# Kernel tuning notes

Hardware: AMD Instinct MI355X
Metric: run time of the kernel (lower is better)

Reference implementation:

```python
import jax, jax.numpy as jnp
import numpy as np
from jax import lax

G, DS, RANK, K = 4, 16, 8, 4  # num_groups, d_state, dt_rank, conv kernel


def setup_inputs() -> dict:
    key = jax.random.key(0)
    B, C, L = 8, 512, 2048
    D = C // G      # per-group dim = 128
    E = 2 * D       # mamba d_inner (expand=2) = 256
    ks = jax.random.split(key, 12)
    rn = lambda k, shape, s=0.02: jax.random.normal(k, shape, jnp.float32) * s
    return {
        "x": jax.random.normal(ks[0], (B, C, L), jnp.float32),
        "gamma": jnp.ones((C,), jnp.float32),
        "beta": jnp.zeros((C,), jnp.float32),
        "cam_w1": rn(ks[1], (C // 4, C)),
        "cam_b1": jnp.zeros((C // 4,), jnp.float32),
        "cam_w2": rn(ks[2], (C, C // 4)),
        "cam_b2": jnp.zeros((C,), jnp.float32),
        "Win": rn(ks[3], (G, 2 * E, D)),
        "convw": rn(ks[4], (G, E, K), 0.1),
        "convb": jnp.zeros((G, E), jnp.float32),
        "Wxp": rn(ks[5], (G, RANK + 2 * DS, E)),
        "Wdt": rn(ks[6], (G, E, RANK), 0.1),
        "bdt": jnp.full((G, E), -4.6, jnp.float32),  # softplus(-4.6) ~ 0.01
        "Alog": jnp.log(jnp.broadcast_to(jnp.arange(1, DS + 1, dtype=jnp.float32), (G, E, DS))),
        "Dp": jnp.ones((G, E), jnp.float32),
        "Wout": rn(ks[7], (G, D, E)),
        "proj_w": rn(ks[8], (C, C)),
        "proj_b": jnp.zeros((C,), jnp.float32),
    }


def _vss_block(x, Win, convw, convb, Wxp, Wdt, bdt, Alog, Dp, Wout):
    """Mamba-style selective-scan block. x: (B, D, L) for one channel group."""
    Bsz, D, L = x.shape
    E = Win.shape[0] // 2
    S = Alog.shape[1]
    xz = jnp.einsum('ed,bdl->bel', Win, x)           # (B, 2E, L)
    xp, z = jnp.split(xz, 2, axis=1)
    # causal depthwise conv (kernel K)
    xpad = jnp.pad(xp, ((0, 0), (0, 0), (K - 1, 0)))
    xc = lax.conv_general_dilated(xpad, convw[:, None, :], (1,), 'VALID',
                                  feature_group_count=E,
                                  dimension_numbers=('NCH', 'OIH', 'NCH'))
    xc = jax.nn.silu(xc + convb[None, :, None])      # (B, E, L)
    xdbl = jnp.einsum('re,bel->brl', Wxp, xc)        # (B, R+2S, L)
    dt_low = xdbl[:, :RANK]
    Bc = xdbl[:, RANK:RANK + S]                      # (B, S, L)
    Cc = xdbl[:, RANK + S:]                          # (B, S, L)
    dt = jax.nn.softplus(jnp.einsum('er,brl->bel', Wdt, dt_low) + bdt[None, :, None])
    A = -jnp.exp(Alog)                               # (E, S)

    def step(h, inp):
        dt_t, B_t, C_t, x_t = inp                    # (B,E),(B,S),(B,S),(B,E)
        h = jnp.exp(dt_t[..., None] * A) * h + (dt_t * x_t)[..., None] * B_t[:, None, :]
        y = jnp.einsum('bes,bs->be', h, C_t)
        return h, y

    seq = (dt.transpose(2, 0, 1), Bc.transpose(2, 0, 1),
           Cc.transpose(2, 0, 1), xc.transpose(2, 0, 1))
    h0 = jnp.zeros((Bsz, E, S), x.dtype)
    _, ys = lax.scan(step, h0, seq)                  # (L, B, E)
    y = ys.transpose(1, 2, 0) + Dp[None, :, None] * xc
    y = y * jax.nn.silu(z)
    return jnp.einsum('de,bel->bdl', Wout, y)        # back to (B, D, L)


def reference(x, gamma, beta, cam_w1, cam_b1, cam_w2, cam_b2, Win, convw, convb,
              Wxp, Wdt, bdt, Alog, Dp, Wout, proj_w, proj_b):
    residual = x
    # LayerNorm over channel dim (torch: transpose -> LN(d_model) -> transpose)
    mu = jnp.mean(x, axis=1, keepdims=True)
    var = jnp.var(x, axis=1, keepdims=True)
    xn = (x - mu) * lax.rsqrt(var + 1e-5) * gamma[None, :, None] + beta[None, :, None]
    # channel attention (CAM): global avg pool over L, two 1x1 convs, sigmoid
    pooled = jnp.mean(xn, axis=2)                                    # (B, C)
    w = jax.nn.sigmoid(jax.nn.relu(pooled @ cam_w1.T + cam_b1) @ cam_w2.T + cam_b2)
    B_, C, L = x.shape
    D = C // G
    xg = xn.reshape(B_, G, D, L).transpose(1, 0, 2, 3)               # (G, B, D, L)
    outs = jax.vmap(_vss_block)(xg, Win, convw, convb, Wxp, Wdt, bdt, Alog, Dp, Wout)
    y = outs.transpose(1, 0, 2, 3).reshape(B_, C, L)                 # concat groups
    y = y * w[:, :, None]
    y = jnp.einsum('oc,bcl->bol', proj_w, y) + proj_b[None, :, None]  # 1x1 conv proj
    return y + residual
```

## Files before the change

kernel.cpp:

```cpp
#include <hip/hip_runtime.h>
#include <hip/hip_bf16.h>
#include <math.h>

#define B_  8
#define C_  512
#define L_  2048
#define G_  4
#define D_  128
#define E_  256
#define S_  16
#define NC_ 64
#define LC_ 32
#define CH_ 128

typedef __hip_bfloat16 bf16;
typedef __attribute__((ext_vector_type(4))) unsigned short ushort4_t;
typedef __attribute__((ext_vector_type(8))) short short8_t;
typedef __attribute__((ext_vector_type(4))) float f32x4;

__device__ __forceinline__ float b2f(bf16 v) { return __bfloat162float(v); }
__device__ __forceinline__ bf16  f2b(float v) { return __float2bfloat16(v); }
__device__ __forceinline__ float us2f(unsigned short u) {
    union { unsigned int i; float f; } c; c.i = ((unsigned int)u) << 16; return c.f;
}
__device__ __forceinline__ unsigned short f2us(float v) {
    bf16 b = f2b(v); return *(unsigned short*)&b;
}

#define OFFB_XN     0ull
#define OFFB_XPC    16777216ull
#define OFFB_XDBL   50331648ull
#define OFFB_HCH    60817408ull
#define OFFB_HALO   78643200ull
#define OFFB_WINB   78692352ull
#define OFFB_WOUTB  79216640ull
#define OFFB_PROJB  79478784ull
#define OFFB_SSUM   80003072ull
#define OFFB_SSQ    80068608ull
#define OFFB_POOL   80134144ull
#define OFFB_W      80150528ull
#define OFFB_DTSUM  0ull
#define OFFB_HALOT  4194304ull

__device__ __forceinline__ float softplusf(float x) {
    return (x > 20.f) ? x : __logf(1.f + __expf(x));
}
__device__ __forceinline__ float sigmoidf_(float x) {
    return 1.f / (1.f + __expf(-x));
}

__global__ __launch_bounds__(256) void k_cast3(const float* __restrict__ w1,
                                               const float* __restrict__ w2,
                                               const float* __restrict__ w3,
                                               bf16* __restrict__ dst) {
    int i = blockIdx.x * 256 + threadIdx.x;
    float v;
    if (i < 262144)      v = w1[i];
    else if (i < 393216) v = w2[i - 262144];
    else                 v = w3[i - 393216];
    dst[i] = f2b(v);
}

__global__ __launch_bounds__(256) void k_ln_stats(const float* __restrict__ x,
                                                  float* __restrict__ ssum,
                                                  float* __restrict__ ssq) {
    const int t = threadIdx.x;
    const int l = blockIdx.x * 256 + t;
    const int c0 = blockIdx.y * 64;
    const int b = blockIdx.z;
    const float* xb = x + (size_t)b * C_ * L_;
    float s = 0.f, q = 0.f;
    #pragma unroll 8
    for (int cc = 0; cc < 64; ++cc) {
        float v = xb[(size_t)(c0 + cc) * L_ + l];
        s += v; q = fmaf(v, v, q);
    }
    atomicAdd(&ssum[b * L_ + l], s);
    atomicAdd(&ssq[b * L_ + l], q);
}

__global__ __launch_bounds__(256) void k_ln_apply(const float* __restrict__ x,
                                                  const float* __restrict__ ssum,
                                                  const float* __restrict__ ssq,
                                                  const float* __restrict__ gamma,
                                                  const float* __restrict__ beta,
                                                  bf16* __restrict__ xn,
                                                  float* __restrict__ pooled) {
    __shared__ float red[256];
    const int t = threadIdx.x;
    const int blk = blockIdx.x;
    const int b = blk >> 9, c = blk & 511;
    const float gm = gamma[c], bt = beta[c];
    const float* xb = x + ((size_t)b * C_ + c) * L_;
    bf16* xnb = xn + ((size_t)b * C_ + c) * L_;
    const float* smb = ssum + b * L_;
    const float* sqb = ssq + b * L_;
    float pacc = 0.f;
    #pragma unroll
    for (int qq = 0; qq < 8; ++qq) {
        const int l = qq * 256 + t;
        const float sm = smb[l], sq = sqb[l];
        const float mu = sm * (1.f / C_);
        const float var = sq * (1.f / C_) - mu * mu;
        const float rs = rsqrtf(var + 1e-5f);
        const float v = (xb[l] - mu) * rs * gm + bt;
        xnb[l] = f2b(v);
        pacc += v;
    }
    red[t] = pacc;
    __syncthreads();
    #pragma unroll
    for (int off = 128; off; off >>= 1) {
        if (t < off) red[t] += red[t + off];
        __syncthreads();
    }
    if (t == 0) pooled[b * C_ + c] = red[0] * (1.f / L_);
}

__global__ __launch_bounds__(256) void k_cam(const float* __restrict__ pooled,
                                             const float* __restrict__ w1,
                                             const float* __restrict__ b1,
                                             const float* __restrict__ w2,
                                             const float* __restrict__ b2,
                                             float* __restrict__ wv) {
    __shared__ float ps[C_];
    __shared__ float h1[128];
    const int b = blockIdx.x, tid = threadIdx.x;
    ps[tid]       = pooled[b * C_ + tid];
    ps[tid + 256] = pooled[b * C_ + tid + 256];
    __syncthreads();
    if (tid < 128) {
        float acc = b1[tid];
        for (int c = 0; c < C_; ++c) acc = fmaf(w1[tid * C_ + c], ps[c], acc);
        h1[tid] = fmaxf(acc, 0.f);
    }
    __syncthreads();
    #pragma unroll
    for (int t = 0; t < 2; ++t) {
        int o = tid + t * 256;
        float acc = b2[o];
        for (int r = 0; r < 128; ++r) acc = fmaf(w2[o * 128 + r], h1[r], acc);
        wv[b * C_ + o] = sigmoidf_(acc);
    }
}

__global__ __launch_bounds__(256) void k_tr_act(const unsigned short* __restrict__ in,
                                                unsigned short* __restrict__ outp,
                                                int R) {
    __shared__ unsigned short tl[64][68];
    const int t = threadIdx.x;
    const int c0 = blockIdx.x * 64;
    const int r0 = blockIdx.y * 64;
    const size_t pofs = (size_t)blockIdx.z * R * 2048;
    const unsigned short* ip = in + pofs;
    unsigned short* op = outp + pofs;
    const int rr = t >> 4, c4 = (t & 15) * 4;
    #pragma unroll
    for (int q = 0; q < 4; ++q) {
        const int row = q * 16 + rr;
        *(ushort4_t*)&tl[row][c4] =
            *(const ushort4_t*)&ip[(size_t)(r0 + row) * 2048 + c0 + c4];
    }
    __syncthreads();
    #pragma unroll
    for (int q = 0; q < 4; ++q) {
        const int cr = q * 16 + rr;
        ushort4_t v;
        v.x = tl[c4 + 0][cr]; v.y = tl[c4 + 1][cr];
        v.z = tl[c4 + 2][cr]; v.w = tl[c4 + 3][cr];
        *(ushort4_t*)&op[(size_t)(c0 + cr) * R + r0 + c4] = v;
    }
}

template <int KD, typename EPI>
__device__ __forceinline__ void mma_tile(const bf16* __restrict__ W,
                                         const bf16* __restrict__ XT,
                                         const int m0, const int l0, EPI epi) {
    __shared__ __align__(16) short Asm[128][40];
    __shared__ __align__(16) short Xsm[128][40];
    const int tid = threadIdx.x;
    const int row = tid >> 1, kh = (tid & 1) * 16;
    const int lane = tid & 63, wid = tid >> 6;
    const int wm = (wid & 1) * 64, wl = (wid >> 1) * 64;
    const int lm = lane & 15, quad = lane >> 4;
    const short* Wg = (const short*)W;
    const short* Xg = (const short*)XT;
    f32x4 acc[4][4];
    #pragma unroll
    for (int i = 0; i < 4; ++i)
        #pragma unroll
        for (int j = 0; j < 4; ++j) acc[i][j] = (f32x4){0.f, 0.f, 0.f, 0.f};

    for (int k0 = 0; k0 < KD; k0 += 32) {
        __syncthreads();
        *(short8_t*)&Asm[row][kh]     = *(const short8_t*)&Wg[(size_t)(m0 + row) * KD + k0 + kh];
        *(short8_t*)&Asm[row][kh + 8] = *(const short8_t*)&Wg[(size_t)(m0 + row) * KD + k0 + kh + 8];
        *(short8_t*)&Xsm[row][kh]     = *(const short8_t*)&Xg[(size_t)(l0 + row) * KD + k0 + kh];
        *(short8_t*)&Xsm[row][kh + 8] = *(const short8_t*)&Xg[(size_t)(l0 + row) * KD + k0 + kh + 8];
        __syncthreads();
        short8_t af[4], bfr[4];
        #pragma unroll
        for (int i = 0; i < 4; ++i)
            af[i] = *(const short8_t*)&Asm[wm + i * 16 + lm][quad * 8];
        #pragma unroll
        for (int j = 0; j < 4; ++j)
            bfr[j] = *(const short8_t*)&Xsm[wl + j * 16 + lm][quad * 8];
        #pragma unroll
        for (int i = 0; i < 4; ++i)
            #pragma unroll
            for (int j = 0; j < 4; ++j)
                acc[i][j] = __builtin_amdgcn_mfma_f32_16x16x32_bf16(af[i], bfr[j], acc[i][j], 0, 0, 0);
    }
    #pragma unroll
    for (int i = 0; i < 4; ++i) {
        #pragma unroll
        for (int j = 0; j < 4; ++j) {
            #pragma unroll
            for (int r = 0; r < 4; ++r) {
                const int m = m0 + wm + i * 16 + quad * 4 + r;
                const int l = l0 + wl + j * 16 + lm;
                epi(m, l, acc[i][j][r]);
            }
        }
    }
}

__global__ __launch_bounds__(256) void k_mm_win(const bf16* __restrict__ winB,
                                                const bf16* __restrict__ xnT,
                                                bf16* __restrict__ xpT,
                                                bf16* __restrict__ zT) {
    const int m0 = blockIdx.x * 128;
    const int l0 = blockIdx.y * 128;
    const int bg = blockIdx.z, g = bg & 3;
    const bf16* A  = xnT + (size_t)bg * L_ * 128;
    const bf16* Bt = winB + (size_t)g * 512 * 128;
    unsigned short* xpb = (unsigned short*)xpT + (size_t)bg * L_ * E_;
    unsigned short* zb  = (unsigned short*)zT  + (size_t)bg * L_ * E_;
    mma_tile<128>(A, Bt, m0, l0,
                  [&](int lr, int ec, float v) {
                      if (ec < 256) xpb[(size_t)lr * E_ + ec] = f2us(v);
                      else          zb[(size_t)lr * E_ + (ec - 256)] = f2us(v);
                  });
}

__global__ __launch_bounds__(256) void k_mm_wout(const bf16* __restrict__ woutB,
                                                 const bf16* __restrict__ yT,
                                                 const float* __restrict__ wvec,
                                                 bf16* __restrict__ scaledT) {
    const int m0 = blockIdx.x * 128;
    const int bg = blockIdx.z, b = bg >> 2, g = bg & 3;
    const bf16* A  = yT + (size_t)bg * L_ * E_;
    const bf16* Bt = woutB + (size_t)g * 128 * 256;
    unsigned short* Outp = (unsigned short*)scaledT + (size_t)b * L_ * C_;
    const float* wrow = wvec + b * C_ + g * D_;
    mma_tile<256>(A, Bt, m0, 0,
                  [&](int lr, int dc, float v) {
                      Outp[(size_t)lr * C_ + g * D_ + dc] = f2us(v * wrow[dc]);
                  });
}

__global__ __launch_bounds__(256) void k_mm_proj(const bf16* __restrict__ projB,
                                                 const bf16* __restrict__ scaledT,
                                                 const float* __restrict__ pb,
                                                 const float* __restrict__ xres,
                                                 float* __restrict__ outp) {
    const int l0 = blockIdx.x * 128, m0 = blockIdx.y * 128;
    const int b = blockIdx.z;
    const bf16* XT = scaledT + (size_t)b * L_ * C_;
    const float* xr = xres + (size_t)b * C_ * L_;
    float* Outp = outp + (size_t)b * C_ * L_;
    mma_tile<512>(projB, XT, m0, l0,
                  [&](int m, int l, float v) {
                      Outp[(size_t)m * L_ + l] = v + pb[m] + xr[(size_t)m * L_ + l];
                  });
}

__global__ __launch_bounds__(256) void k_halo(const bf16* __restrict__ xpT,
                                              bf16* __restrict__ halo) {
    const int c = blockIdx.x, bg = blockIdx.y, e = threadIdx.x;
    if (c == 0) return;
    const unsigned short* src = (const unsigned short*)xpT +
                                ((size_t)bg * L_ + c * CH_ - 3) * E_ + e;
    unsigned short* dst = (unsigned short*)halo + ((size_t)(bg * 16 + c) * 3) * E_ + e;
    #pragma unroll
    for (int j = 0; j < 3; ++j) dst[j * E_] = src[(size_t)j * E_];
}

__global__ __launch_bounds__(256) void k_conv(bf16* __restrict__ xpT,
                                              const bf16* __restrict__ halo,
                                              const float* __restrict__ convw,
                                              const float* __restrict__ convb) {
    const int c = blockIdx.x, bg = blockIdx.y;
    const int e = threadIdx.x;
    const int g = bg & 3;
    const int ge = g * E_ + e;
    unsigned short* row = (unsigned short*)xpT + ((size_t)bg * L_ + c * CH_) * E_ + e;
    float x3, x2, x1;
    if (c == 0) { x3 = 0.f; x2 = 0.f; x1 = 0.f; }
    else {
        const unsigned short* hp = (const unsigned short*)halo +
                                   ((size_t)(bg * 16 + c) * 3) * E_ + e;
        x3 = us2f(hp[0]); x2 = us2f(hp[E_]); x1 = us2f(hp[2 * E_]);
    }
    const float w0 = convw[ge * 4 + 0], w1 = convw[ge * 4 + 1],
                w2 = convw[ge * 4 + 2], w3 = convw[ge * 4 + 3];
    const float bb = convb[ge];
    #pragma unroll 4
    for (int l = 0; l < CH_; ++l) {
        const float xv = us2f(row[(size_t)l * E_]);
        float acc = bb;
        acc = fmaf(w0, x3, acc);
        acc = fmaf(w1, x2, acc);
        acc = fmaf(w2, x1, acc);
        acc = fmaf(w3, xv, acc);
        row[(size_t)l * E_] = f2us(acc * sigmoidf_(acc));
        x3 = x2; x2 = x1; x1 = xv;
    }
}

__global__ __launch_bounds__(256) void k_xdbl(const float* __restrict__ Wxp,
                                              const bf16* __restrict__ xcT,
                                              float* __restrict__ xdbl) {
    __shared__ unsigned short xs[32][258];
    __shared__ float wsm[40][256];
    const int tid = threadIdx.x;
    const int l0 = blockIdx.x * 32;
    const int bg = blockIdx.y;
    const int g = bg & 3;
    const float* wsrc = Wxp + g * (40 * 256);
    for (int i = tid; i < 40 * 256; i += 256) wsm[i >> 8][i & 255] = wsrc[i];
    const unsigned short* xcu = (const unsigned short*)xcT + ((size_t)bg * L_ + l0) * E_;
    #pragma unroll
    for (int it = 0; it < 16; ++it) {
        const int flat = it * 256 + tid;
        const int li = flat >> 7, e2 = (flat & 127) * 2;
        *(unsigned int*)&xs[li][e2] = *(const unsigned int*)&xcu[(size_t)li * E_ + e2];
    }
    __syncthreads();
    const int li = tid & 31, rg = tid >> 5;
    float acc[5];
    #pragma unroll
    for (int j = 0; j < 5; ++j) acc[j] = 0.f;
    for (int k4 = 0; k4 < 64; ++k4) {
        const int k = k4 * 4;
        const float xv0 = us2f(xs[li][k + 0]);
        const float xv1 = us2f(xs[li][k + 1]);
        const float xv2 = us2f(xs[li][k + 2]);
        const float xv3 = us2f(xs[li][k + 3]);
        #pragma unroll
        for (int j = 0; j < 5; ++j) {
            const float4 wq = *reinterpret_cast<const float4*>(&wsm[rg * 5 + j][k]);
            acc[j] = fmaf(wq.x, xv0, fmaf(wq.y, xv1, fmaf(wq.z, xv2, fmaf(wq.w, xv3, acc[j]))));
        }
    }
    float* ob = xdbl + ((size_t)bg * L_ + l0 + li) * 40 + rg * 5;
    #pragma unroll
    for (int j = 0; j < 5; ++j) ob[j] = acc[j];
}

__global__ __launch_bounds__(256) void k_scanA(const float* __restrict__ xdbl,
                                               const bf16* __restrict__ xcT,
                                               const float* __restrict__ Wdt,
                                               const float* __restrict__ bdt,
                                               const float* __restrict__ Alog,
                                               bf16* __restrict__ hch,
                                               float* __restrict__ dtsum) {
    __shared__ float ts[LC_][28];
    const int tid = threadIdx.x;
    const int blk = blockIdx.x;
    const int bg = blk >> 6, ch = blk & 63;
    const int g = bg & 3;
    const int l0 = ch * LC_;
    const int eg = tid;

    const unsigned short* xr = (const unsigned short*)xcT +
                               ((size_t)bg * L_ + l0) * E_ + eg;
    unsigned short xcur[8], xnxt[8];
    #pragma unroll
    for (int k = 0; k < 8; ++k) xcur[k] = xr[(size_t)k * E_];

    float wdtv[8];
    #pragma unroll
    for (int r = 0; r < 8; ++r) wdtv[r] = Wdt[(g * E_ + eg) * 8 + r];
    const float bde = bdt[g * E_ + eg];
    const float a0 = -__expf(Alog[(g * E_ + eg) * 16]);

    {
        const float* xd = xdbl + ((size_t)bg * L_ + l0) * 40;
        const int li = tid & 31, r0 = (tid >> 5) * 3;
        #pragma unroll
        for (int r = 0; r < 3; ++r) ts[li][r0 + r] = xd[(size_t)li * 40 + r0 + r];
    }
    __syncthreads();

    float h[16];
    #pragma unroll
    for (int s = 0; s < 16; ++s) h[s] = 0.f;
    float dsum = 0.f;

    #pragma unroll 1
    for (int qw = 0; qw < 4; ++qw) {
        if (qw < 3) {
            const unsigned short* xp2 = xr + (size_t)(qw + 1) * 8 * E_;
            #pragma unroll
            for (int k = 0; k < 8; ++k) xnxt[k] = xp2[(size_t)k * E_];
        }
        #pragma unroll
        for (int k = 0; k < 8; ++k) {
            const int i = qw * 8 + k;
            const float4 d0 = *reinterpret_cast<const float4*>(&ts[i][0]);
            const float4 d1 = *reinterpret_cast<const float4*>(&ts[i][4]);
            float dtp = bde;
            dtp = fmaf(wdtv[0], d0.x, dtp); dtp = fmaf(wdtv[1], d0.y, dtp);
            dtp = fmaf(wdtv[2], d0.z, dtp); dtp = fmaf(wdtv[3], d0.w, dtp);
            dtp = fmaf(wdtv[4], d1.x, dtp); dtp = fmaf(wdtv[5], d1.y, dtp);
            dtp = fmaf(wdtv[6], d1.z, dtp); dtp = fmaf(wdtv[7], d1.w, dtp);
            const float dt = softplusf(dtp);
            const float xv = us2f(xcur[k]);
            const float dtx = dt * xv;
            dsum += dt;
            const float p  = __expf(dt * a0);
            const float p2 = p * p;
            const float p4 = p2 * p2;
            float wa = p, wb = p2, wc = p2 * p, wd = p4;
            #pragma unroll
            for (int gq = 0; gq < 4; ++gq) {
                const float4 bq = *reinterpret_cast<const float4*>(&ts[i][8 + gq * 4]);
                float* hp = &h[gq * 4];
                hp[0] = fmaf(wa, hp[0], dtx * bq.x);
                hp[1] = fmaf(wb, hp[1], dtx * bq.y);
                hp[2] = fmaf(wc, hp[2], dtx * bq.z);
                hp[3] = fmaf(wd, hp[3], dtx * bq.w);
                if (gq < 3) { wa *= p4; wb *= p4; wc *= p4; wd *= p4; }
            }
        }
        #pragma unroll
        for (int k = 0; k < 8; ++k) xcur[k] = xnxt[k];
    }
    unsigned short* hb = (unsigned short*)hch + ((size_t)(bg * NC_ + ch) * E_ + eg) * 16;
    #pragma unroll
    for (int q = 0; q < 4; ++q) {
        ushort4_t v;
        v.x = f2us(h[q * 4 + 0]); v.y = f2us(h[q * 4 + 1]);
        v.z = f2us(h[q * 4 + 2]); v.w = f2us(h[q * 4 + 3]);
        *(ushort4_t*)&hb[q * 4] = v;
    }
    dtsum[(bg * NC_ + ch) * E_ + eg] = dsum;
}

__global__ __launch_bounds__(256) void k_scanB(bf16* hbuf,
                                               const float* __restrict__ dtsum,
                                               const float* __restrict__ Alog) {
    const int t = blockIdx.x * 256 + threadIdx.x;
    const int s = t & 15;
    const int e = (t >> 4) & 255;
    const int bg = t >> 12;
    const int g = bg & 3;
    const float a = -__expf(Alog[(g * E_ + e) * 16 + s]);
    float h = 0.f;
    for (int c = 0; c < NC_; ++c) {
        const int idx = (bg * NC_ + c) * E_ + e;
        const float hc = b2f(hbuf[(size_t)idx * 16 + s]);
        hbuf[(size_t)idx * 16 + s] = f2b(h);
        h = fmaf(__expf(a * dtsum[idx]), h, hc);
    }
}

__global__ __launch_bounds__(256) void k_scanC(const float* __restrict__ xdbl,
                                               const bf16* __restrict__ xcT,
                                               bf16* __restrict__ zy,
                                               const float* __restrict__ Wdt,
                                               const float* __restrict__ bdt,
                                               const float* __restrict__ Alog,
                                               const float* __restrict__ Dp,
                                               const bf16* __restrict__ hin) {
    __shared__ float ts[LC_][44];
    const int tid = threadIdx.x;
    const int blk = blockIdx.x;
    const int bg = blk >> 6, ch = blk & 63;
    const int g = bg & 3;
    const int l0 = ch * LC_;
    const int eg = tid;

    const unsigned short* xr = (const unsigned short*)xcT +
                               ((size_t)bg * L_ + l0) * E_ + eg;
    unsigned short* zr = (unsigned short*)zy + ((size_t)bg * L_ + l0) * E_ + eg;
    unsigned short xcur[8], xnxt[8], zcur[8], znxt[8];
    #pragma unroll
    for (int k = 0; k < 8; ++k) { xcur[k] = xr[(size_t)k * E_]; zcur[k] = zr[(size_t)k * E_]; }

    float wdtv[8];
    #pragma unroll
    for (int r = 0; r < 8; ++r) wdtv[r] = Wdt[(g * E_ + eg) * 8 + r];
    const float bde = bdt[g * E_ + eg];
    const float a0 = -__expf(Alog[(g * E_ + eg) * 16]);
    const float dpe = Dp[g * E_ + eg];
    float h[16];
    const unsigned short* hib = (const unsigned short*)hin +
                                ((size_t)(bg * NC_ + ch) * E_ + eg) * 16;
    #pragma unroll
    for (int q = 0; q < 4; ++q) {
        const ushort4_t hv = *(const ushort4_t*)&hib[q * 4];
        h[q * 4 + 0] = us2f(hv.x); h[q * 4 + 1] = us2f(hv.y);
        h[q * 4 + 2] = us2f(hv.z); h[q * 4 + 3] = us2f(hv.w);
    }

    {
        const float* xd = xdbl + ((size_t)bg * L_ + l0) * 40;
        const int li = tid & 31, r0 = (tid >> 5) * 5;
        #pragma unroll
        for (int r = 0; r < 5; ++r) ts[li][r0 + r] = xd[(size_t)li * 40 + r0 + r];
    }
    __syncthreads();

    #pragma unroll 1
    for (int qw = 0; qw < 4; ++qw) {
        if (qw < 3) {
            const unsigned short* xp2 = xr + (size_t)(qw + 1) * 8 * E_;
            const unsigned short* zp2 = zr + (size_t)(qw + 1) * 8 * E_;
            #pragma unroll
            for (int k = 0; k < 8; ++k) { xnxt[k] = xp2[(size_t)k * E_]; znxt[k] = zp2[(size_t)k * E_]; }
        }
        #pragma unroll
        for (int k = 0; k < 8; ++k) {
            const int i = qw * 8 + k;
            const float4 d0 = *reinterpret_cast<const float4*>(&ts[i][0]);
            const float4 d1 = *reinterpret_cast<const float4*>(&ts[i][4]);
            float dtp = bde;
            dtp = fmaf(wdtv[0], d0.x, dtp); dtp = fmaf(wdtv[1], d0.y, dtp);
            dtp = fmaf(wdtv[2], d0.z, dtp); dtp = fmaf(wdtv[3], d0.w, dtp);
            dtp = fmaf(wdtv[4], d1.x, dtp); dtp = fmaf(wdtv[5], d1.y, dtp);
            dtp = fmaf(wdtv[6], d1.z, dtp); dtp = fmaf(wdtv[7], d1.w, dtp);
            const float dt = softplusf(dtp);
            const float xv = us2f(xcur[k]);
            const float dtx = dt * xv;
            const float p  = __expf(dt * a0);
            const float p2 = p * p;
            const float p4 = p2 * p2;
            float wa = p, wb = p2, wc = p2 * p, wd = p4;
            float yv0 = 0.f, yv1 = 0.f, yv2 = 0.f, yv3 = 0.f;
            #pragma unroll
            for (int gq = 0; gq < 4; ++gq) {
                const float4 bq = *reinterpret_cast<const float4*>(&ts[i][8 + gq * 4]);
                const float4 cq = *reinterpret_cast<const float4*>(&ts[i][24 + gq * 4]);
                float* hp = &h[gq * 4];
                hp[0] = fmaf(wa, hp[0], dtx * bq.x); yv0 = fmaf(hp[0], cq.x, yv0);
                hp[1] = fmaf(wb, hp[1], dtx * bq.y); yv1 = fmaf(hp[1], cq.y, yv1);
                hp[2] = fmaf(wc, hp[2], dtx * bq.z); yv2 = fmaf(hp[2], cq.z, yv2);
                hp[3] = fmaf(wd, hp[3], dtx * bq.w); yv3 = fmaf(hp[3], cq.w, yv3);
                if (gq < 3) { wa *= p4; wb *= p4; wc *= p4; wd *= p4; }
            }
            float yv = (yv0 + yv1) + (yv2 + yv3);
            yv = fmaf(dpe, xv, yv);
            const float zv = us2f(zcur[k]);
            yv *= zv * sigmoidf_(zv);
            zr[(size_t)i * E_] = f2us(yv);
        }
        #pragma unroll
        for (int k = 0; k < 8; ++k) { xcur[k] = xnxt[k]; zcur[k] = znxt[k]; }
    }
}

extern "C" void kernel_launch(void* const* d_in, const int* in_sizes, int n_in,
                              void* d_out, int out_size, void* d_ws, size_t ws_size,
                              hipStream_t stream) {
    const float* x      = (const float*)d_in[0];
    const float* gamma  = (const float*)d_in[1];
    const float* beta   = (const float*)d_in[2];
    const float* cam_w1 = (const float*)d_in[3];
    const float* cam_b1 = (const float*)d_in[4];
    const float* cam_w2 = (const float*)d_in[5];
    const float* cam_b2 = (const float*)d_in[6];
    const float* Win    = (const float*)d_in[7];
    const float* convw  = (const float*)d_in[8];
    const float* convb  = (const float*)d_in[9];
    const float* Wxp    = (const float*)d_in[10];
    const float* Wdt    = (const float*)d_in[11];
    const float* bdt    = (const float*)d_in[12];
    const float* Alog   = (const float*)d_in[13];
    const float* Dp     = (const float*)d_in[14];
    const float* Wout   = (const float*)d_in[15];
    const float* proj_w = (const float*)d_in[16];
    const float* proj_b = (const float*)d_in[17];
    float* outp = (float*)d_out;
    char* ws = (char*)d_ws;

    bf16*  xn      = (bf16*) (ws + OFFB_XN);
    bf16*  xpT     = (bf16*) (ws + OFFB_XPC);
    float* xdblT   = (float*)(ws + OFFB_XDBL);
    bf16*  hbuf    = (bf16*) (ws + OFFB_HCH);
    float* dtsums  = (float*)(ws + OFFB_DTSUM);
    bf16*  haloT   = (bf16*) (ws + OFFB_HALOT);
    bf16*  winB    = (bf16*) (ws + OFFB_WINB);
    bf16*  woutB   = (bf16*) (ws + OFFB_WOUTB);
    bf16*  projB   = (bf16*) (ws + OFFB_PROJB);
    float* ssum    = (float*)(ws + OFFB_SSUM);
    float* ssq     = (float*)(ws + OFFB_SSQ);
    float* pooled  = (float*)(ws + OFFB_POOL);
    float* wbuf    = (float*)(ws + OFFB_W);
    bf16*  xnT     = (bf16*) (ws + OFFB_HCH);
    bf16*  scaledT = (bf16*) (ws + OFFB_HCH);
    bf16*  zyT     = (bf16*) d_out;

    hipMemsetAsync(ssum, 0, 2 * B_ * L_ * sizeof(float), stream);

    k_cast3<<<2560, 256, 0, stream>>>(Win, Wout, proj_w, winB);

    k_ln_stats<<<dim3(8, 8, 8), 256, 0, stream>>>(x, ssum, ssq);
    k_ln_apply<<<4096, 256, 0, stream>>>(x, ssum, ssq, gamma, beta, xn, pooled);
    k_cam<<<8, 256, 0, stream>>>(pooled, cam_w1, cam_b1, cam_w2, cam_b2, wbuf);

    k_tr_act<<<dim3(32, 2, 32), 256, 0, stream>>>((const unsigned short*)xn,
                                                  (unsigned short*)xnT, 128);
    k_mm_win<<<dim3(16, 4, 32), 256, 0, stream>>>(winB, xnT, xpT, zyT);
    k_halo<<<dim3(16, 32), 256, 0, stream>>>(xpT, haloT);
    k_conv<<<dim3(16, 32), 256, 0, stream>>>(xpT, haloT, convw, convb);
    k_xdbl<<<dim3(64, 32), 256, 0, stream>>>(Wxp, xpT, xdblT);
    k_scanA<<<B_ * G_ * NC_, 256, 0, stream>>>(xdblT, xpT, Wdt, bdt, Alog, hbuf, dtsums);
    k_scanB<<<512, 256, 0, stream>>>(hbuf, dtsums, Alog);
    k_scanC<<<B_ * G_ * NC_, 256, 0, stream>>>(xdblT, xpT, zyT, Wdt, bdt, Alog, Dp, hbuf);

    k_mm_wout<<<dim3(16, 1, 32), 256, 0, stream>>>(woutB, zyT, wbuf, scaledT);
    k_mm_proj<<<dim3(16, 4, 8), 256, 0, stream>>>(projB, scaledT, proj_b, x, outp);
}
```

Measured before the change: 391.9 us.

## Fuse LayerNorm apply with transpose and use direct global-to-LDS loads in GEMM tiles

The LayerNorm apply kernel now writes its normalized output directly in the transposed (L-major per group) layout through an LDS tile, and accumulates pooled sums with atomics. This removes the separate transpose kernel and one bf16 round-trip of the activation through global memory. Separately, the shared GEMM tile loader switches to global_load_lds 16-byte loads into an unpadded LDS layout, which skips the register staging but may add LDS bank conflicts because the row padding is gone. The memset is extended to zero the pooled buffer, which assumes it sits right after ssum and ssq.

```diff
diff --git a/kernel.cpp b/kernel.cpp
--- a/kernel.cpp
+++ b/kernel.cpp
@@ -25,6 +25,12 @@
 }
 __device__ __forceinline__ unsigned short f2us(float v) {
     bf16 b = f2b(v); return *(unsigned short*)&b;
+}
+
+__device__ __forceinline__ void gload16(const void* g, void* l) {
+    __builtin_amdgcn_global_load_lds(
+        (const __attribute__((address_space(1))) void*)g,
+        (__attribute__((address_space(3))) void*)l, 16, 0, 0);
 }
 
 #define OFFB_XN     0ull
@@ -79,42 +85,57 @@
     atomicAdd(&ssq[b * L_ + l], q);
 }
 
-__global__ __launch_bounds__(256) void k_ln_apply(const float* __restrict__ x,
-                                                  const float* __restrict__ ssum,
-                                                  const float* __restrict__ ssq,
-                                                  const float* __restrict__ gamma,
-                                                  const float* __restrict__ beta,
-                                                  bf16* __restrict__ xn,
-                                                  float* __restrict__ pooled) {
-    __shared__ float red[256];
+__global__ __launch_bounds__(256) void k_lnT(const float* __restrict__ x,
+                                             const float* __restrict__ ssum,
+                                             const float* __restrict__ ssq,
+                                             const float* __restrict__ gamma,
+                                             const float* __restrict__ beta,
+                                             unsigned short* __restrict__ xnT,
+                                             float* __restrict__ pooled) {
+    __shared__ unsigned short tl[64][68];
+    __shared__ float mus[64], rss[64];
     const int t = threadIdx.x;
-    const int blk = blockIdx.x;
-    const int b = blk >> 9, c = blk & 511;
-    const float gm = gamma[c], bt = beta[c];
-    const float* xb = x + ((size_t)b * C_ + c) * L_;
-    bf16* xnb = xn + ((size_t)b * C_ + c) * L_;
-    const float* smb = ssum + b * L_;
-    const float* sqb = ssq + b * L_;
-    float pacc = 0.f;
-    #pragma unroll
-    for (int qq = 0; qq < 8; ++qq) {
-        const int l = qq * 256 + t;
-        const float sm = smb[l], sq = sqb[l];
+    const int l0 = blockIdx.x * 64;
+    const int c0 = blockIdx.y * 64;
+    const int b = blockIdx.z;
+    if (t < 64) {
+        const float sm = ssum[b * L_ + l0 + t], sq = ssq[b * L_ + l0 + t];
         const float mu = sm * (1.f / C_);
         const float var = sq * (1.f / C_) - mu * mu;
-        const float rs = rsqrtf(var + 1e-5f);
-        const float v = (xb[l] - mu) * rs * gm + bt;
-        xnb[l] = f2b(v);
-        pacc += v;
-    }
-    red[t] = pacc;
+        mus[t] = mu; rss[t] = rsqrtf(var + 1e-5f);
+    }
     __syncthreads();
-    #pragma unroll
-    for (int off = 128; off; off >>= 1) {
-        if (t < off) red[t] += red[t + off];
-        __syncthreads();
-    }
-    if (t == 0) pooled[b * C_ + c] = red[0] * (1.f / L_);
+    const int rr = t >> 4, c4 = (t & 15) * 4;
+    const float* xb = x + ((size_t)b * C_ + c0) * L_ + l0;
+    #pragma unroll
+    for (int q = 0; q < 4; ++q) {
+        const int row = q * 16 + rr;
+        const float gm = gamma[c0 + row], bt = beta[c0 + row];
+        const float4 xv = *(const float4*)&xb[(size_t)row * L_ + c4];
+        ushort4_t o;
+        o.x = f2us((xv.x - mus[c4 + 0]) * rss[c4 + 0] * gm + bt);
+        o.y = f2us((xv.y - mus[c4 + 1]) * rss[c4 + 1] * gm + bt);
+        o.z = f2us((xv.z - mus[c4 + 2]) * rss[c4 + 2] * gm + bt);
+        o.w = f2us((xv.w - mus[c4 + 3]) * rss[c4 + 3] * gm + bt);
+        *(ushort4_t*)&tl[row][c4] = o;
+    }
+    __syncthreads();
+    const int g = c0 >> 7, eoff = c0 & 127;
+    unsigned short* op = xnT + (size_t)(b * 4 + g) * L_ * 128;
+    #pragma unroll
+    for (int q = 0; q < 4; ++q) {
+        const int cr = q * 16 + rr;
+        ushort4_t v;
+        v.x = tl[c4 + 0][cr]; v.y = tl[c4 + 1][cr];
+        v.z = tl[c4 + 2][cr]; v.w = tl[c4 + 3][cr];
+        *(ushort4_t*)&op[(size_t)(l0 + cr) * 128 + eoff + c4] = v;
+    }
+    if (t < 64) {
+        float s = 0.f;
+        #pragma unroll
+        for (int l = 0; l < 64; ++l) s += us2f(tl[t][l]);
+        atomicAdd(&pooled[b * C_ + c0 + t], s);
+    }
 }
 
 __global__ __launch_bounds__(256) void k_cam(const float* __restrict__ pooled,
@@ -126,8 +147,8 @@
     __shared__ float ps[C_];
     __shared__ float h1[128];
     const int b = blockIdx.x, tid = threadIdx.x;
-    ps[tid]       = pooled[b * C_ + tid];
-    ps[tid + 256] = pooled[b * C_ + tid + 256];
+    ps[tid]       = pooled[b * C_ + tid] * (1.f / L_);
+    ps[tid + 256] = pooled[b * C_ + tid + 256] * (1.f / L_);
     __syncthreads();
     if (tid < 128) {
         float acc = b1[tid];
@@ -144,47 +165,19 @@
     }
 }
 
-__global__ __launch_bounds__(256) void k_tr_act(const unsigned short* __restrict__ in,
-                                                unsigned short* __restrict__ outp,
-                                                int R) {
-    __shared__ unsigned short tl[64][68];
-    const int t = threadIdx.x;
-    const int c0 = blockIdx.x * 64;
-    const int r0 = blockIdx.y * 64;
-    const size_t pofs = (size_t)blockIdx.z * R * 2048;
-    const unsigned short* ip = in + pofs;
-    unsigned short* op = outp + pofs;
-    const int rr = t >> 4, c4 = (t & 15) * 4;
-    #pragma unroll
-    for (int q = 0; q < 4; ++q) {
-        const int row = q * 16 + rr;
-        *(ushort4_t*)&tl[row][c4] =
-            *(const ushort4_t*)&ip[(size_t)(r0 + row) * 2048 + c0 + c4];
-    }
-    __syncthreads();
-    #pragma unroll
-    for (int q = 0; q < 4; ++q) {
-        const int cr = q * 16 + rr;
-        ushort4_t v;
-        v.x = tl[c4 + 0][cr]; v.y = tl[c4 + 1][cr];
-        v.z = tl[c4 + 2][cr]; v.w = tl[c4 + 3][cr];
-        *(ushort4_t*)&op[(size_t)(c0 + cr) * R + r0 + c4] = v;
-    }
-}
-
 template <int KD, typename EPI>
 __device__ __forceinline__ void mma_tile(const bf16* __restrict__ W,
                                          const bf16* __restrict__ XT,
                                          const int m0, const int l0, EPI epi) {
-    __shared__ __align__(16) short Asm[128][40];
-    __shared__ __align__(16) short Xsm[128][40];
+    __shared__ __align__(16) short Asm[128 * 32];
+    __shared__ __align__(16) short Xsm[128 * 32];
     const int tid = threadIdx.x;
-    const int row = tid >> 1, kh = (tid & 1) * 16;
     const int lane = tid & 63, wid = tid >> 6;
     const int wm = (wid & 1) * 64, wl = (wid >> 1) * 64;
     const int lm = lane & 15, quad = lane >> 4;
     const short* Wg = (const short*)W;
     const short* Xg = (const short*)XT;
+    const int row0 = tid >> 2, kc0 = (tid & 3) * 8;
     f32x4 acc[4][4];
     #pragma unroll
     for (int i = 0; i < 4; ++i)
@@ -193,18 +186,20 @@
 
     for (int k0 = 0; k0 < KD; k0 += 32) {
         __syncthreads();
-        *(short8_t*)&Asm[row][kh]     = *(const short8_t*)&Wg[(size_t)(m0 + row) * KD + k0 + kh];
-        *(short8_t*)&Asm[row][kh + 8] = *(const short8_t*)&Wg[(size_t)(m0 + row) * KD + k0 + kh + 8];
-        *(short8_t*)&Xsm[row][kh]     = *(const short8_t*)&Xg[(size_t)(l0 + row) * KD + k0 + kh];
-        *(short8_t*)&Xsm[row][kh + 8] = *(const short8_t*)&Xg[(size_t)(l0 + row) * KD + k0 + kh + 8];
+        const size_t aofs = (size_t)(m0 + row0) * KD + k0 + kc0;
+        const size_t xofs = (size_t)(l0 + row0) * KD + k0 + kc0;
+        gload16(&Wg[aofs],                 &Asm[tid * 8]);
+        gload16(&Wg[aofs + (size_t)64 * KD], &Asm[(256 + tid) * 8]);
+        gload16(&Xg[xofs],                 &Xsm[tid * 8]);
+        gload16(&Xg[xofs + (size_t)64 * KD], &Xsm[(256 + tid) * 8]);
         __syncthreads();
         short8_t af[4], bfr[4];
         #pragma unroll
         for (int i = 0; i < 4; ++i)
-            af[i] = *(const short8_t*)&Asm[wm + i * 16 + lm][quad * 8];
+            af[i] = *(const short8_t*)&Asm[(wm + i * 16 + lm) * 32 + quad * 8];
         #pragma unroll
         for (int j = 0; j < 4; ++j)
-            bfr[j] = *(const short8_t*)&Xsm[wl + j * 16 + lm][quad * 8];
+            bfr[j] = *(const short8_t*)&Xsm[(wl + j * 16 + lm) * 32 + quad * 8];
         #pragma unroll
         for (int i = 0; i < 4; ++i)
             #pragma unroll
@@ -585,7 +580,6 @@
     float* outp = (float*)d_out;
     char* ws = (char*)d_ws;
 
-    bf16*  xn      = (bf16*) (ws + OFFB_XN);
     bf16*  xpT     = (bf16*) (ws + OFFB_XPC);
     float* xdblT   = (float*)(ws + OFFB_XDBL);
     bf16*  hbuf    = (bf16*) (ws + OFFB_HCH);
@@ -602,16 +596,15 @@
     bf16*  scaledT = (bf16*) (ws + OFFB_HCH);
     bf16*  zyT     = (bf16*) d_out;
 
-    hipMemsetAsync(ssum, 0, 2 * B_ * L_ * sizeof(float), stream);
+    hipMemsetAsync(ssum, 0, 2 * B_ * L_ * sizeof(float) + B_ * C_ * sizeof(float), stream);
 
     k_cast3<<<2560, 256, 0, stream>>>(Win, Wout, proj_w, winB);
 
     k_ln_stats<<<dim3(8, 8, 8), 256, 0, stream>>>(x, ssum, ssq);
-    k_ln_apply<<<4096, 256, 0, stream>>>(x, ssum, ssq, gamma, beta, xn, pooled);
+    k_lnT<<<dim3(32, 8, 8), 256, 0, stream>>>(x, ssum, ssq, gamma, beta,
+                                              (unsigned short*)xnT, pooled);
     k_cam<<<8, 256, 0, stream>>>(pooled, cam_w1, cam_b1, cam_w2, cam_b2, wbuf);
 
-    k_tr_act<<<dim3(32, 2, 32), 256, 0, stream>>>((const unsigned short*)xn,
-                                                  (unsigned short*)xnT, 128);
     k_mm_win<<<dim3(16, 4, 32), 256, 0, stream>>>(winB, xnT, xpT, zyT);
     k_halo<<<dim3(16, 32), 256, 0, stream>>>(xpT, haloT);
     k_conv<<<dim3(16, 32), 256, 0, stream>>>(xpT, haloT, convw, convb);
```

Measured after the change: 369.6 us. -5.7%, faster.
